# Optimization experiments

Measured on AMD Instinct MI355X. Metric: run time of the kernel, lower is better.

## Reference

```python
import jax, jax.numpy as jnp
import numpy as np

B, T, H, K = 64, 1024, 256, 4  # batch, seq_len, hidden_dim, crf_size


def setup_inputs() -> dict:
    key = jax.random.key(0)
    ks = jax.random.split(key, 8)
    return {
        "sentence_features": jax.random.normal(ks[0], (B, T, H), dtype=jnp.float32),
        "conv_w": jax.random.normal(ks[1], (H, H, 3), dtype=jnp.float32) * (1.0 / np.sqrt(3 * H)),
        "conv_b": jnp.zeros((H,), dtype=jnp.float32),
        "lin_w": jax.random.normal(ks[2], (K, H), dtype=jnp.float32) * (1.0 / np.sqrt(H)),
        "lin_b": jnp.zeros((K,), dtype=jnp.float32),
        "crf_start": jax.random.uniform(ks[3], (K,), dtype=jnp.float32, minval=-0.1, maxval=0.1),
        "crf_end": jax.random.uniform(ks[4], (K,), dtype=jnp.float32, minval=-0.1, maxval=0.1),
        "crf_trans": jax.random.uniform(ks[5], (K, K), dtype=jnp.float32, minval=-0.1, maxval=0.1),
    }


def _emissions(x, conv_w, conv_b, lin_w, lin_b):
    # x: [B, T, H] -> transpose -> Conv1d(k=3, pad=1) -> ReLU -> transpose -> Linear
    xc = jnp.swapaxes(x, 1, 2)  # [B, H, T]
    y = jax.lax.conv_general_dilated(
        xc, conv_w, window_strides=(1,), padding=((1, 1),),
        dimension_numbers=("NCH", "OIH", "NCH"))
    y = jax.nn.relu(y + conv_b[None, :, None])
    y = jnp.swapaxes(y, 1, 2)  # [B, T, H]
    return y @ lin_w.T + lin_b  # [B, T, K]


def _viterbi_decode(em, start, end, trans):
    # em: [B, T, K]; torchcrf CRF.decode with no mask (batch_first=True)
    score0 = start[None, :] + em[:, 0]  # [B, K]

    def step(score, emit_t):
        # score [B, K] over prev tag; broadcast to [B, K_prev, K_next]
        nxt = score[:, :, None] + trans[None, :, :] + emit_t[:, None, :]
        return jnp.max(nxt, axis=1), jnp.argmax(nxt, axis=1)  # new score, best prev tag

    em_rest = jnp.swapaxes(em[:, 1:], 0, 1)  # [T-1, B, K]
    final, history = jax.lax.scan(step, score0, em_rest)
    final = final + end[None, :]
    last_tag = jnp.argmax(final, axis=-1)  # [B]

    def back(tag, idx_t):
        prev = jnp.take_along_axis(idx_t, tag[:, None], axis=1)[:, 0]
        return prev, prev

    _, tags_head = jax.lax.scan(back, last_tag, history, reverse=True)  # [T-1, B]
    path = jnp.concatenate([jnp.swapaxes(tags_head, 0, 1), last_tag[:, None]], axis=1)
    return path.astype(jnp.int32)  # [B, T]


def reference(sentence_features, conv_w, conv_b, lin_w, lin_b, crf_start, crf_end, crf_trans):
    em = _emissions(sentence_features, conv_w, conv_b, lin_w, lin_b)
    return _viterbi_decode(em, crf_start, crf_end, crf_trans)
```

## Files before the change

kernel.cpp:

```cpp
#include <hip/hip_runtime.h>
#include <cstdint>
#include <cstddef>

typedef __attribute__((ext_vector_type(8))) short short8;
typedef __attribute__((ext_vector_type(4))) float f32x4;

constexpr int Bn = 64, Tn = 1024, Hn = 256, Kn = 4;
constexpr int TT = 128;
constexpr int AROWS = TT + 2;
constexpr int ARSTR = 144;

__device__ __forceinline__ unsigned bf16rne(float f) {
  unsigned u = __float_as_uint(f);
  return (u + 0x7fffu + ((u >> 16) & 1u)) >> 16;
}

__global__ __launch_bounds__(256) void pack_b_k(const float* __restrict__ conv_w,
                                                unsigned short* __restrict__ Bp) {
  int gt = blockIdx.x * 256 + threadIdx.x;
  int fid = gt >> 6, l = gt & 63;
  int ks = fid >> 5, rem = fid & 31;
  int p = rem >> 4, nf = rem & 15;
  int n = nf * 16 + (l & 15);
  int k0 = ks * 32 + ((l >> 4) << 3);
  short8 s;
  #pragma unroll
  for (int j = 0; j < 8; ++j) {
    int k = k0 + j;
    int dt = k >> 8, i = k & 255;
    float w = conv_w[n * 768 + i * 3 + dt];
    unsigned hb = bf16rne(w);
    if (p == 0) s[j] = (short)hb;
    else        s[j] = (short)bf16rne(w - __uint_as_float(hb << 16));
  }
  *reinterpret_cast<short8*>(Bp + (size_t)fid * 512 + l * 8) = s;
}

__device__ __forceinline__ void gload_lds16(const void* g, void* l) {
  __builtin_amdgcn_global_load_lds(
      (const __attribute__((address_space(1))) void*)g,
      (__attribute__((address_space(3))) void*)l, 16, 0, 0);
}

__global__ __launch_bounds__(256, 3) void emis_k(const float* __restrict__ x,
    const unsigned short* __restrict__ Bp, const float* __restrict__ conv_b,
    const float* __restrict__ lin_w, float* __restrict__ em2) {
  __shared__ __align__(16) char A_lds[AROWS * ARSTR];
  __shared__ __align__(16) char B_lds[2 * 16 * 1024];

  const int b = blockIdx.z, ny = blockIdx.y, t0 = blockIdx.x * TT;
  const int tid = threadIdx.x, lane = tid & 63, w = tid >> 6;
  const int wm = w >> 1, wn = w & 1;
  const int nf0 = ny * 8;
  const float* xb = x + (size_t)b * Tn * Hn;

  auto stageA = [&](int ig) {
    #pragma unroll 1
    for (int it = 0; it < 5; ++it) {
      int idx = it * 256 + tid;
      if (idx < AROWS * 8) {
        int row = idx >> 3, c4 = idx & 7;
        int trow = t0 - 1 + row;
        float4 v = make_float4(0.f, 0.f, 0.f, 0.f);
        if (trow >= 0 && trow < Tn)
          v = *reinterpret_cast<const float4*>(xb + (size_t)trow * Hn + ig * 32 + c4 * 4);
        unsigned h[4], lo[4];
        float vf[4] = {v.x, v.y, v.z, v.w};
        #pragma unroll
        for (int q = 0; q < 4; ++q) {
          h[q] = bf16rne(vf[q]);
          lo[q] = bf16rne(vf[q] - __uint_as_float(h[q] << 16));
        }
        uint2 hp, lp;
        hp.x = h[0] | (h[1] << 16);  hp.y = h[2] | (h[3] << 16);
        lp.x = lo[0] | (lo[1] << 16); lp.y = lo[2] | (lo[3] << 16);
        char* base = A_lds + row * ARSTR + c4 * 8;
        *reinterpret_cast<uint2*>(base) = hp;
        *reinterpret_cast<uint2*>(base + 64) = lp;
      }
    }
  };

  auto stageB = [&](int sel, int ks) {
    #pragma unroll
    for (int q = 0; q < 4; ++q) {
      int fi = w * 4 + q;
      int p = fi >> 3, nfl = fi & 7;
      const char* src = reinterpret_cast<const char*>(Bp)
          + ((size_t)((ks * 2 + p) * 16 + nf0 + nfl)) * 1024 + lane * 16;
      char* dst = B_lds + sel * 16384 + fi * 1024 + lane * 16;
      gload_lds16(src, dst);
    }
  };

  f32x4 acc[4][4];
  #pragma unroll
  for (int mf = 0; mf < 4; ++mf)
    #pragma unroll
    for (int nf = 0; nf < 4; ++nf) acc[mf][nf] = (f32x4)0.f;

  const char* aB = A_lds + (lane & 15) * ARSTR + ((lane >> 4) << 4) + wm * 64 * ARSTR;
  const char* bB = B_lds + lane * 16 + wn * 4096;

  stageB(0, 0);
  stageA(0);
  __syncthreads();

  int sel = 0;
  #pragma unroll 1
  for (int ig = 0; ig < 8; ++ig) {
    #pragma unroll 1
    for (int dt = 0; dt < 3; ++dt) {
      const int ks = dt * 8 + ig;
      const int nks = (dt < 2) ? ks + 8 : (ig < 7 ? ig + 1 : -1);
      if (nks >= 0) stageB(sel ^ 1, nks);

      short8 Bh[4], Bl[4];
      #pragma unroll
      for (int nf = 0; nf < 4; ++nf) {
        Bh[nf] = *reinterpret_cast<const short8*>(bB + sel * 16384 + nf * 1024);
        Bl[nf] = *reinterpret_cast<const short8*>(bB + sel * 16384 + 8192 + nf * 1024);
      }
      #pragma unroll
      for (int mf = 0; mf < 4; ++mf) {
        const char* ap = aB + (mf * 16 + dt) * ARSTR;
        short8 Ah = *reinterpret_cast<const short8*>(ap);
        short8 Al = *reinterpret_cast<const short8*>(ap + 64);
        #pragma unroll
        for (int nf = 0; nf < 4; ++nf) {
          f32x4 c = acc[mf][nf];
          c = __builtin_amdgcn_mfma_f32_16x16x32_bf16(Ah, Bh[nf], c, 0, 0, 0);
          c = __builtin_amdgcn_mfma_f32_16x16x32_bf16(Al, Bh[nf], c, 0, 0, 0);
          c = __builtin_amdgcn_mfma_f32_16x16x32_bf16(Ah, Bl[nf], c, 0, 0, 0);
          c = __builtin_amdgcn_mfma_f32_16x16x32_bf16(Al, Bl[nf], c, 0, 0, 0);
          acc[mf][nf] = c;
        }
      }
      if (dt == 2 && ig < 7) { __syncthreads(); stageA(ig + 1); }
      __syncthreads();
      sel ^= 1;
    }
  }

  f32x4 pem[4][4];
  #pragma unroll
  for (int mf = 0; mf < 4; ++mf)
    #pragma unroll
    for (int v = 0; v < 4; ++v) pem[mf][v] = (f32x4)0.f;

  #pragma unroll
  for (int nf = 0; nf < 4; ++nf) {
    const int gcol = ny * 128 + wn * 64 + nf * 16 + (lane & 15);
    const float cb = conv_b[gcol];
    f32x4 lw;
    lw[0] = lin_w[gcol]; lw[1] = lin_w[256 + gcol];
    lw[2] = lin_w[512 + gcol]; lw[3] = lin_w[768 + gcol];
    #pragma unroll
    for (int mf = 0; mf < 4; ++mf)
      #pragma unroll
      for (int v = 0; v < 4; ++v) {
        float val = fmaxf(acc[mf][nf][v] + cb, 0.f);
        pem[mf][v] += val * lw;
      }
  }
  #pragma unroll
  for (int mf = 0; mf < 4; ++mf)
    #pragma unroll
    for (int v = 0; v < 4; ++v) {
      f32x4 t = pem[mf][v];
      #pragma unroll
      for (int m = 1; m < 16; m <<= 1) {
        f32x4 q;
        q[0] = __shfl_xor(t[0], m); q[1] = __shfl_xor(t[1], m);
        q[2] = __shfl_xor(t[2], m); q[3] = __shfl_xor(t[3], m);
        t += q;
      }
      pem[mf][v] = t;
    }
  float* red = reinterpret_cast<float*>(A_lds);
  if ((lane & 15) == 0) {
    const int g = lane >> 4;
    #pragma unroll
    for (int mf = 0; mf < 4; ++mf)
      #pragma unroll
      for (int v = 0; v < 4; ++v) {
        int r = wm * 64 + mf * 16 + g * 4 + v;
        *reinterpret_cast<f32x4*>(red + (r * 2 + wn) * 4) = pem[mf][v];
      }
  }
  __syncthreads();
  if (tid < 128) {
    f32x4 s0 = *reinterpret_cast<f32x4*>(red + tid * 8);
    f32x4 s1 = *reinterpret_cast<f32x4*>(red + tid * 8 + 4);
    f32x4 s = s0 + s1;
    *reinterpret_cast<f32x4*>(em2 + ((size_t)(b * Tn + t0 + tid) * 2 + ny) * 4) = s;
  }
}

__device__ __forceinline__ unsigned int compose_map(unsigned int a, unsigned int b) {
#if __has_builtin(__builtin_amdgcn_perm)
  return __builtin_amdgcn_perm(a, a, b);
#else
  unsigned int c = 0;
  #pragma unroll
  for (int k = 0; k < 4; ++k) {
    unsigned int sel = (b >> (8 * k)) & 0xffu;
    c |= ((a >> (8 * sel)) & 0xffu) << (8 * k);
  }
  return c;
#endif
}

template <int J>
__device__ __forceinline__ float qb(float v) {
  return __int_as_float(__builtin_amdgcn_update_dpp(
      0, __float_as_int(v), (J * 0x55), 0xf, 0xf, true));
}

#define PSTEP(EV, T)                                                       \
  {                                                                        \
    shf[((T) - 1) * 4 + kk] = s;                                           \
    float c0 = qb<0>(s) + trc0;                                            \
    float c1 = qb<1>(s) + trc1;                                            \
    float c2 = qb<2>(s) + trc2;                                            \
    float c3 = qb<3>(s) + trc3;                                            \
    s = fmaxf(fmaxf(c0, c1), fmaxf(c2, c3)) + (EV);                        \
  }

__global__ __launch_bounds__(64) void viterbi_k(const float* __restrict__ em2,
    const float* __restrict__ lin_b, const float* __restrict__ cstart,
    const float* __restrict__ cend, const float* __restrict__ ctrans,
    int* __restrict__ out) {
  __shared__ float4 se[Tn];
  __shared__ float4 sh[Tn - 1];
  __shared__ int s_last;
  const int b = blockIdx.x, lane = threadIdx.x;
  const float4* e2 = reinterpret_cast<const float4*>(em2 + (size_t)b * Tn * 8);
  const float lb0 = lin_b[0], lb1 = lin_b[1], lb2 = lin_b[2], lb3 = lin_b[3];
  for (int i = lane; i < Tn; i += 64) {
    float4 a = e2[i * 2], c = e2[i * 2 + 1];
    se[i] = make_float4(a.x + c.x + lb0, a.y + c.y + lb1,
                        a.z + c.z + lb2, a.w + c.w + lb3);
  }
  float tr[4][4];
  #pragma unroll
  for (int j = 0; j < 4; ++j)
    #pragma unroll
    for (int k = 0; k < 4; ++k) tr[j][k] = ctrans[j * 4 + k];
  __syncthreads();

  if (lane < 4) {
    const int kk = lane;
    const float* sef = reinterpret_cast<const float*>(se);
    float* shf = reinterpret_cast<float*>(sh);
    const float trc0 = ctrans[0 * 4 + kk];
    const float trc1 = ctrans[1 * 4 + kk];
    const float trc2 = ctrans[2 * 4 + kk];
    const float trc3 = ctrans[3 * 4 + kk];
    float s = cstart[kk] + sef[kk];
    float e[8];
    #pragma unroll
    for (int d = 0; d < 8; ++d) e[d] = sef[(1 + d) * 4 + kk];
    int t = 1;
    #pragma unroll 1
    for (int g = 0; g < 127; ++g, t += 8) {
      float f[8];
      #pragma unroll
      for (int d = 0; d < 8; ++d) f[d] = e[d];
      #pragma unroll
      for (int d = 0; d < 8; ++d) e[d] = sef[(t + 8 + d) * 4 + kk];
      PSTEP(f[0], t);     PSTEP(f[1], t + 1);
      PSTEP(f[2], t + 2); PSTEP(f[3], t + 3);
      PSTEP(f[4], t + 4); PSTEP(f[5], t + 5);
      PSTEP(f[6], t + 6); PSTEP(f[7], t + 7);
    }
    PSTEP(e[0], 1017); PSTEP(e[1], 1018); PSTEP(e[2], 1019);
    PSTEP(e[3], 1020); PSTEP(e[4], 1021); PSTEP(e[5], 1022);
    PSTEP(e[6], 1023);
    s += cend[kk];
    float f0 = __shfl(s, 0), f1 = __shfl(s, 1);
    float f2 = __shfl(s, 2), f3 = __shfl(s, 3);
    if (kk == 0) {
      int tag = 0; float bf = f0;
      if (f1 > bf) { bf = f1; tag = 1; }
      if (f2 > bf) { bf = f2; tag = 2; }
      if (f3 > bf) { bf = f3; tag = 3; }
      s_last = tag;
    }
  }
  __syncthreads();

  const unsigned int ID = 0x03020100u;
  unsigned int mloc[16];
  const int t0 = lane * 16;
  #pragma unroll
  for (int k = 0; k < 16; ++k) {
    const int t = t0 + k;
    if (t < Tn - 1) {
      const float4 s = sh[t];
      const float4 e = se[t + 1];
      const float sj[4] = {s.x, s.y, s.z, s.w};
      const float ev[4] = {e.x, e.y, e.z, e.w};
      unsigned int mw = 0;
      #pragma unroll
      for (int kk = 0; kk < 4; ++kk) {
        float best = (sj[0] + tr[0][kk]) + ev[kk];
        int bi = 0;
        #pragma unroll
        for (int j = 1; j < 4; ++j) {
          float cc = (sj[j] + tr[j][kk]) + ev[kk];
          if (cc > best) { best = cc; bi = j; }
        }
        mw |= (unsigned)bi << (8 * kk);
      }
      mloc[k] = mw;
    } else {
      mloc[k] = ID;
    }
  }
  unsigned int P = mloc[15];
  #pragma unroll
  for (int k = 14; k >= 0; --k) P = compose_map(mloc[k], P);
  #pragma unroll
  for (int d = 1; d < 64; d <<= 1) {
    unsigned int q = (unsigned int)__shfl_down((int)P, d);
    if (lane + d > 63) q = ID;
    P = compose_map(P, q);
  }
  unsigned int E = (unsigned int)__shfl_down((int)P, 1);
  if (lane == 63) E = ID;
  const int last = s_last;
  unsigned int tag = (E >> (8 * last)) & 3u;
  int* ob = out + (size_t)b * Tn;
  #pragma unroll
  for (int k = 15; k >= 0; --k) {
    tag = (mloc[k] >> (8 * tag)) & 3u;
    ob[t0 + k] = (int)tag;
  }
}

extern "C" void kernel_launch(void* const* d_in, const int* in_sizes, int n_in,
                              void* d_out, int out_size, void* d_ws, size_t ws_size,
                              hipStream_t stream) {
  const float* x      = (const float*)d_in[0];
  const float* conv_w = (const float*)d_in[1];
  const float* conv_b = (const float*)d_in[2];
  const float* lin_w  = (const float*)d_in[3];
  const float* lin_b  = (const float*)d_in[4];
  const float* cstart = (const float*)d_in[5];
  const float* cend   = (const float*)d_in[6];
  const float* ctrans = (const float*)d_in[7];
  int* out = (int*)d_out;

  unsigned short* Bp = (unsigned short*)d_ws;
  float* em2 = (float*)((char*)d_ws + 786432);

  pack_b_k<<<192, 256, 0, stream>>>(conv_w, Bp);
  emis_k<<<dim3(Tn / TT, 2, Bn), 256, 0, stream>>>(x, Bp, conv_b, lin_w, em2);
  viterbi_k<<<Bn, 64, 0, stream>>>(em2, lin_b, cstart, cend, ctrans, out);
}
```

Before: 148.4 us.

## Load conv weights straight to registers, drop lo*lo MFMA term, prefetch across steps

The B-operand LDS double buffer and its async global-to-LDS copies are removed. Each wave now loads its weight fragments directly from global memory into registers, prefetching the next k-step while the current one runs on MFMA. The loop is unrolled over pairs of input groups, which removes the per-step barriers, and s_setprio raises priority around the MFMA block. The Al*Bl product in the split-bf16 scheme is dropped, cutting MFMAs by a quarter at a small precision cost. A barrier is added before the reduction reuses A_lds.

```diff
diff --git a/kernel.cpp b/kernel.cpp
--- a/kernel.cpp
+++ b/kernel.cpp
@@ -36,22 +36,14 @@
   *reinterpret_cast<short8*>(Bp + (size_t)fid * 512 + l * 8) = s;
 }
 
-__device__ __forceinline__ void gload_lds16(const void* g, void* l) {
-  __builtin_amdgcn_global_load_lds(
-      (const __attribute__((address_space(1))) void*)g,
-      (__attribute__((address_space(3))) void*)l, 16, 0, 0);
-}
-
 __global__ __launch_bounds__(256, 3) void emis_k(const float* __restrict__ x,
     const unsigned short* __restrict__ Bp, const float* __restrict__ conv_b,
     const float* __restrict__ lin_w, float* __restrict__ em2) {
   __shared__ __align__(16) char A_lds[AROWS * ARSTR];
-  __shared__ __align__(16) char B_lds[2 * 16 * 1024];
 
   const int b = blockIdx.z, ny = blockIdx.y, t0 = blockIdx.x * TT;
   const int tid = threadIdx.x, lane = tid & 63, w = tid >> 6;
   const int wm = w >> 1, wn = w & 1;
-  const int nf0 = ny * 8;
   const float* xb = x + (size_t)b * Tn * Hn;
 
   auto stageA = [&](int ig) {
@@ -81,15 +73,13 @@
     }
   };
 
-  auto stageB = [&](int sel, int ks) {
-    #pragma unroll
-    for (int q = 0; q < 4; ++q) {
-      int fi = w * 4 + q;
-      int p = fi >> 3, nfl = fi & 7;
-      const char* src = reinterpret_cast<const char*>(Bp)
-          + ((size_t)((ks * 2 + p) * 16 + nf0 + nfl)) * 1024 + lane * 16;
-      char* dst = B_lds + sel * 16384 + fi * 1024 + lane * 16;
-      gload_lds16(src, dst);
+  const char* bsrc = reinterpret_cast<const char*>(Bp)
+      + (size_t)(ny * 8 + wn * 4) * 1024 + lane * 16;
+  auto loadB = [&](short8* Bh, short8* Bl, int ks) {
+    #pragma unroll
+    for (int nf = 0; nf < 4; ++nf) {
+      Bh[nf] = *reinterpret_cast<const short8*>(bsrc + (size_t)((ks * 2 + 0) * 16 + nf) * 1024);
+      Bl[nf] = *reinterpret_cast<const short8*>(bsrc + (size_t)((ks * 2 + 1) * 16 + nf) * 1024);
     }
   };
 
@@ -100,47 +90,52 @@
     for (int nf = 0; nf < 4; ++nf) acc[mf][nf] = (f32x4)0.f;
 
   const char* aB = A_lds + (lane & 15) * ARSTR + ((lane >> 4) << 4) + wm * 64 * ARSTR;
-  const char* bB = B_lds + lane * 16 + wn * 4096;
-
-  stageB(0, 0);
+
+#define STEP(DT, BH, BL, NBH, NBL, KSN)                                       \
+  {                                                                           \
+    loadB(NBH, NBL, (KSN));                                                   \
+    __builtin_amdgcn_s_setprio(1);                                            \
+    _Pragma("unroll")                                                         \
+    for (int mf = 0; mf < 4; ++mf) {                                          \
+      const char* ap = aB + (mf * 16 + (DT)) * ARSTR;                         \
+      short8 Ah = *reinterpret_cast<const short8*>(ap);                       \
+      short8 Al = *reinterpret_cast<const short8*>(ap + 64);                  \
+      _Pragma("unroll")                                                       \
+      for (int nf = 0; nf < 4; ++nf) {                                        \
+        f32x4 c = acc[mf][nf];                                                \
+        c = __builtin_amdgcn_mfma_f32_16x16x32_bf16(Ah, BH[nf], c, 0, 0, 0);  \
+        c = __builtin_amdgcn_mfma_f32_16x16x32_bf16(Al, BH[nf], c, 0, 0, 0);  \
+        c = __builtin_amdgcn_mfma_f32_16x16x32_bf16(Ah, BL[nf], c, 0, 0, 0);  \
+        acc[mf][nf] = c;                                                      \
+      }                                                                       \
+    }                                                                         \
+    __builtin_amdgcn_s_setprio(0);                                            \
+  }
+
+  short8 BhA[4], BlA[4], BhB[4], BlB[4];
+  loadB(BhA, BlA, 0);
   stageA(0);
   __syncthreads();
 
-  int sel = 0;
   #pragma unroll 1
-  for (int ig = 0; ig < 8; ++ig) {
-    #pragma unroll 1
-    for (int dt = 0; dt < 3; ++dt) {
-      const int ks = dt * 8 + ig;
-      const int nks = (dt < 2) ? ks + 8 : (ig < 7 ? ig + 1 : -1);
-      if (nks >= 0) stageB(sel ^ 1, nks);
-
-      short8 Bh[4], Bl[4];
-      #pragma unroll
-      for (int nf = 0; nf < 4; ++nf) {
-        Bh[nf] = *reinterpret_cast<const short8*>(bB + sel * 16384 + nf * 1024);
-        Bl[nf] = *reinterpret_cast<const short8*>(bB + sel * 16384 + 8192 + nf * 1024);
-      }
-      #pragma unroll
-      for (int mf = 0; mf < 4; ++mf) {
-        const char* ap = aB + (mf * 16 + dt) * ARSTR;
-        short8 Ah = *reinterpret_cast<const short8*>(ap);
-        short8 Al = *reinterpret_cast<const short8*>(ap + 64);
-        #pragma unroll
-        for (int nf = 0; nf < 4; ++nf) {
-          f32x4 c = acc[mf][nf];
-          c = __builtin_amdgcn_mfma_f32_16x16x32_bf16(Ah, Bh[nf], c, 0, 0, 0);
-          c = __builtin_amdgcn_mfma_f32_16x16x32_bf16(Al, Bh[nf], c, 0, 0, 0);
-          c = __builtin_amdgcn_mfma_f32_16x16x32_bf16(Ah, Bl[nf], c, 0, 0, 0);
-          c = __builtin_amdgcn_mfma_f32_16x16x32_bf16(Al, Bl[nf], c, 0, 0, 0);
-          acc[mf][nf] = c;
-        }
-      }
-      if (dt == 2 && ig < 7) { __syncthreads(); stageA(ig + 1); }
+  for (int igp = 0; igp < 4; ++igp) {
+    const int ig0 = igp * 2, ig1 = ig0 + 1;
+    STEP(0, BhA, BlA, BhB, BlB, 8 + ig0);
+    STEP(1, BhB, BlB, BhA, BlA, 16 + ig0);
+    STEP(2, BhA, BlA, BhB, BlB, ig1);
+    __syncthreads();
+    stageA(ig1);
+    __syncthreads();
+    STEP(0, BhB, BlB, BhA, BlA, 8 + ig1);
+    STEP(1, BhA, BlA, BhB, BlB, 16 + ig1);
+    STEP(2, BhB, BlB, BhA, BlA, (ig1 < 7 ? ig1 + 1 : 0));
+    if (igp < 3) {
       __syncthreads();
-      sel ^= 1;
-    }
-  }
+      stageA(ig1 + 1);
+      __syncthreads();
+    }
+  }
+#undef STEP
 
   f32x4 pem[4][4];
   #pragma unroll
@@ -177,6 +172,7 @@
       }
       pem[mf][v] = t;
     }
+  __syncthreads();
   float* red = reinterpret_cast<float*>(A_lds);
   if ((lane & 15) == 0) {
     const int g = lane >> 4;
```

New measurement: 134.0 us. 1.11x faster.
